# Kernel optimization log

Measured on AMD Instinct MI355X. Metric: run time of the kernel, lower is better.

## Reference

```python
import jax, jax.numpy as jnp
import numpy as np

B, N, CIN, H, OUT, E = 64, 512, 128, 256, 12, 8192


def setup_inputs() -> dict:
    key = jax.random.key(0)
    ks = jax.random.split(key, 32)
    g = lambda i, shape, s=0.05: jax.random.normal(ks[i], shape, jnp.float32) * s
    inp = {
        "x": jax.random.normal(ks[0], (B, N, CIN), jnp.float32),
        "edge_index": jax.random.randint(ks[1], (2, E), 0, N),
        "edge_weight": jax.random.uniform(ks[2], (E,), dtype=jnp.float32),
    }
    # TGCN2 gate params: GCNConv lin (CIN->H, bias added after aggregation) + Linear(2H->H)
    for j, gate in enumerate(["z", "r", "h"]):
        base = 3 + j * 4
        inp[f"W{gate}"] = g(base, (CIN, H))
        inp[f"b{gate}"] = jnp.zeros((H,), jnp.float32)
        inp[f"l{gate}_W"] = g(base + 1, (2 * H, H))
        inp[f"l{gate}_b"] = jnp.zeros((H,), jnp.float32)
    # 2-layer GRU (torch layout: W_ih [3H,in], W_hh [3H,H]); eval mode (dropout off)
    inp["Wih0"] = g(16, (3 * H, CIN)); inp["Whh0"] = g(17, (3 * H, H))
    inp["bih0"] = jnp.zeros((3 * H,), jnp.float32); inp["bhh0"] = jnp.zeros((3 * H,), jnp.float32)
    inp["Wih1"] = g(18, (3 * H, H)); inp["Whh1"] = g(19, (3 * H, H))
    inp["bih1"] = jnp.zeros((3 * H,), jnp.float32); inp["bhh1"] = jnp.zeros((3 * H,), jnp.float32)
    # heads (stored as [in,out] so y = x @ W + b, matching torch x @ W.T + b)
    inp["l1_W"] = g(20, (H, 1)); inp["l1_b"] = jnp.zeros((1,), jnp.float32)
    inp["l2_W"] = g(21, (H, 1)); inp["l2_b"] = jnp.zeros((1,), jnp.float32)
    inp["l3_W"] = g(22, (2, OUT)); inp["l3_b"] = jnp.zeros((OUT,), jnp.float32)
    return inp


def _gcn_norm(edge_index, edge_weight, n_nodes):
    # improved=True -> self loops with fill value 2.0; sym normalization
    loop = jnp.arange(n_nodes)
    src = jnp.concatenate([edge_index[0], loop])
    tgt = jnp.concatenate([edge_index[1], loop])
    ew = jnp.concatenate([edge_weight, jnp.full((n_nodes,), 2.0, edge_weight.dtype)])
    deg = jax.ops.segment_sum(ew, tgt, num_segments=n_nodes)
    dinv = jnp.where(deg > 0, deg ** -0.5, 0.0)
    return src, tgt, dinv[src] * ew * dinv[tgt]


def _gcn_conv(x, W, b, src, tgt, norm):
    xw = x @ W                                   # [B,N,H]
    msg = xw[:, src, :] * norm[None, :, None]    # gather from sources [B,E+N,H]
    out = jnp.zeros_like(xw).at[:, tgt, :].add(msg)  # scatter-add to targets
    return out + b


def _gru_layer(x_sbf, Wih, Whh, bih, bhh):
    h_dim = Whh.shape[1]
    h0 = jnp.zeros((x_sbf.shape[1], h_dim), x_sbf.dtype)

    def step(h, xt):
        gi = xt @ Wih.T + bih
        gh = h @ Whh.T + bhh
        ir, iz, inn = jnp.split(gi, 3, axis=-1)
        hr, hz, hn = jnp.split(gh, 3, axis=-1)
        r = jax.nn.sigmoid(ir + hr)
        z = jax.nn.sigmoid(iz + hz)
        n = jnp.tanh(inn + r * hn)
        h_new = (1.0 - z) * n + z * h
        return h_new, h_new

    _, ys = jax.lax.scan(step, h0, x_sbf)
    return ys  # [S,B,H]


def reference(x, edge_index, edge_weight, Wz, bz, lz_W, lz_b, Wr, br, lr_W, lr_b,
              Wh, bh, lh_W, lh_b, Wih0, Whh0, bih0, bhh0, Wih1, Whh1, bih1, bhh1,
              l1_W, l1_b, l2_W, l2_b, l3_W, l3_b):
    n_nodes = x.shape[1]
    # GRU branch (node dim treated as sequence, as in the source)
    xs = jnp.transpose(x, (1, 0, 2))             # [N,B,CIN]
    h1 = _gru_layer(xs, Wih0, Whh0, bih0, bhh0)
    h2 = _gru_layer(h1, Wih1, Whh1, bih1, bhh1)
    temp = jnp.transpose(h2, (1, 0, 2))          # [B,N,H]
    gru_out = temp @ l2_W + l2_b                 # [B,N,1]
    # TGCN2 cell with H0 = 0
    src, tgt, norm = _gcn_norm(edge_index, edge_weight, n_nodes)
    Hst = jnp.zeros((x.shape[0], n_nodes, lz_W.shape[1]), x.dtype)
    cz = _gcn_conv(x, Wz, bz, src, tgt, norm)
    Z = jax.nn.sigmoid(jnp.concatenate([cz, Hst], axis=2) @ lz_W + lz_b)
    cr = _gcn_conv(x, Wr, br, src, tgt, norm)
    R = jax.nn.sigmoid(jnp.concatenate([cr, Hst], axis=2) @ lr_W + lr_b)
    ch = _gcn_conv(x, Wh, bh, src, tgt, norm)
    H_tilde = jnp.tanh(jnp.concatenate([ch, Hst * R], axis=2) @ lh_W + lh_b)
    Hn = Z * Hst + (1.0 - Z) * H_tilde           # [B,N,H]
    h = jax.nn.relu(Hn) @ l1_W + l1_b            # [B,N,1]
    cat = jnp.concatenate([gru_out, h], axis=2)  # [B,N,2]
    return cat @ l3_W + l3_b                     # [B,N,OUT]
```

## Files before the change

### kernel.cpp

```cpp
#include <hip/hip_runtime.h>


typedef unsigned short u16;
typedef unsigned long long u64;
typedef short s8v __attribute__((ext_vector_type(8)));
typedef float f4v __attribute__((ext_vector_type(4)));

#define NBATCH 64
#define NNODE  512
#define DCIN   128
#define DHID   256
#define NEDGE  8192
#define RING   8
#define SLOTU16 16384

__device__ __forceinline__ u16 f2b(float f) {
    union { float f; unsigned int i; } v; v.f = f;
    unsigned int x = v.i;
    return (u16)((x + 0x7FFFu + ((x >> 16) & 1u)) >> 16);
}
__device__ __forceinline__ float sigm(float x)  { return 1.0f / (1.0f + __expf(-x)); }
__device__ __forceinline__ float tanh_(float x) { return 1.0f - 2.0f / (1.0f + __expf(2.0f * x)); }
__device__ __forceinline__ f4v mfma16(s8v a, s8v b, f4v c) {
    return __builtin_amdgcn_mfma_f32_16x16x32_bf16(a, b, c, 0, 0, 0);
}
__device__ __forceinline__ s8v ld_ring(const u64* p) {
    union { u64 d[2]; s8v v; } u;
    u.d[0] = __hip_atomic_load(p,     __ATOMIC_RELAXED, __HIP_MEMORY_SCOPE_AGENT);
    u.d[1] = __hip_atomic_load(p + 1, __ATOMIC_RELAXED, __HIP_MEMORY_SCOPE_AGENT);
    return u.v;
}
__device__ __forceinline__ void st_ring(u64* p, s8v v) {
    union { s8v v; u64 d[2]; } u; u.v = v;
    __hip_atomic_store(p,     u.d[0], __ATOMIC_RELAXED, __HIP_MEMORY_SCOPE_AGENT);
    __hip_atomic_store(p + 1, u.d[1], __ATOMIC_RELAXED, __HIP_MEMORY_SCOPE_AGENT);
}
__device__ __forceinline__ void wait_joint(const int* f, int tgtf,
                                           const int* g, int tgtg, int l) {
    while (true) {
        int v = 0x7fffffff, tg = -0x7fffffff;
        if (l < 16)      { v = __hip_atomic_load(f + l, __ATOMIC_RELAXED, __HIP_MEMORY_SCOPE_AGENT); tg = tgtf; }
        else if (l < 32) { v = __hip_atomic_load(g + (l - 16), __ATOMIC_RELAXED, __HIP_MEMORY_SCOPE_AGENT); tg = tgtg; }
        if (__all(v >= tg)) break;
        __builtin_amdgcn_s_sleep(2);
    }
    asm volatile("" ::: "memory");
}
__device__ __forceinline__ void wait_one(const int* f, int tgt, int l) {
    while (true) {
        int v = 0x7fffffff;
        if (l < 16) v = __hip_atomic_load(f + l, __ATOMIC_RELAXED, __HIP_MEMORY_SCOPE_AGENT);
        if (__all(v >= tgt)) break;
        __builtin_amdgcn_s_sleep(2);
    }
    asm volatile("" ::: "memory");
}
__device__ __forceinline__ s8v cvt8(const float* p) {
    s8v r;
    #pragma unroll
    for (int e = 0; e < 8; ++e) r[e] = (short)f2b(p[e]);
    return r;
}

__global__ void init_kernel(float* deg, int* counts, int* flags) {
    int i = blockIdx.x * blockDim.x + threadIdx.x;
    if (i < NNODE) { deg[i] = 2.0f; counts[i] = 1; }
    if (i < 128) flags[i] = 0;
}

__global__ void edge_deg_kernel(const int* __restrict__ ei, const float* __restrict__ ew,
                                float* deg, int* counts) {
    int e = blockIdx.x * blockDim.x + threadIdx.x;
    if (e < NEDGE) {
        int t = ei[NEDGE + e];
        atomicAdd(&deg[t], ew[e]);
        atomicAdd(&counts[t], 1);
    }
}

__global__ void scan_kernel(const float* __restrict__ deg, const int* __restrict__ counts,
                            float* __restrict__ dinv, int* __restrict__ rowptr,
                            int* __restrict__ cursor, int* __restrict__ col,
                            float* __restrict__ val) {
    __shared__ int sc[NNODE];
    int i = threadIdx.x;
    float d = deg[i];
    float di = (d > 0.0f) ? (1.0f / sqrtf(d)) : 0.0f;
    dinv[i] = di;
    int cnt = counts[i];
    sc[i] = cnt;
    __syncthreads();
    for (int ofs = 1; ofs < NNODE; ofs <<= 1) {
        int add = (i >= ofs) ? sc[i - ofs] : 0;
        __syncthreads();
        sc[i] += add;
        __syncthreads();
    }
    int ex = sc[i] - cnt;
    rowptr[i] = ex;
    if (i == NNODE - 1) rowptr[NNODE] = sc[NNODE - 1];
    col[ex] = i;
    val[ex] = di * 2.0f * di;
    cursor[i] = ex + 1;
}

__global__ void fill_kernel(const int* __restrict__ ei, const float* __restrict__ ew,
                            const float* __restrict__ dinv, int* cursor,
                            int* __restrict__ col, float* __restrict__ val) {
    int e = blockIdx.x * blockDim.x + threadIdx.x;
    if (e < NEDGE) {
        int s = ei[e], t = ei[NEDGE + e];
        int p = atomicAdd(&cursor[t], 1);
        col[p] = s;
        val[p] = dinv[s] * ew[e] * dinv[t];
    }
}

__global__ void fold_kernel(const float* __restrict__ Wz, const float* __restrict__ lzW,
                            const float* __restrict__ bz, const float* __restrict__ lzb,
                            const float* __restrict__ Wh, const float* __restrict__ lhW,
                            const float* __restrict__ bh, const float* __restrict__ lhb,
                            u16* __restrict__ Wf, float* __restrict__ bfold) {
    int nidx = blockIdx.x;
    int g = nidx & 1, j = nidx >> 1;
    int k = threadIdx.x;
    const float* W = g ? Wh : Wz;
    const float* L = g ? lhW : lzW;
    float acc = 0.0f;
    for (int m = 0; m < DHID; ++m)
        acc += W[k * DHID + m] * L[m * DHID + j];
    Wf[nidx * DCIN + k] = f2b(acc);
    if (k == 0) {
        const float* bg = g ? bh : bz;
        const float* lb = g ? lhb : lzb;
        float ab = 0.0f;
        for (int m = 0; m < DHID; ++m) ab += bg[m] * L[m * DHID + j];
        bfold[nidx] = ab + lb[j];
    }
}

__global__ void repack_w_kernel(const float* __restrict__ Wih, const float* __restrict__ Whh,
                                int KCX, int KC, int KX, int KH, u16* __restrict__ dst) {
    int id = blockIdx.x * 256 + threadIdx.x;
    int total = 16 * KC * 3 * 64;
    if (id >= total) return;
    int l = id & 63; int rest = id >> 6;
    int g = rest % 3; rest /= 3;
    int kc = rest % KC; rest /= KC;
    int r = rest;
    int j = r * 16 + (l & 15);
    int q = l >> 4;
    const float* src; int k;
    if (kc < KCX) { src = Wih + (size_t)(g * 256 + j) * KX; k = kc * 32 + q * 8; }
    else          { src = Whh + (size_t)(g * 256 + j) * KH; k = (kc - KCX) * 32 + q * 8; }
    u16* d = dst + (((size_t)(r * KC + kc)) * 3 + g) * 512 + l * 8;
    #pragma unroll
    for (int e = 0; e < 8; ++e) d[e] = f2b(src[k + e]);
}

__global__ __launch_bounds__(256)
void tgcn_kernel(const float* __restrict__ x, const int* __restrict__ rowptr,
                 const int* __restrict__ col, const float* __restrict__ val,
                 const u16* __restrict__ Wf, const float* __restrict__ bfold,
                 const float* __restrict__ l1W, float* __restrict__ hdot) {
    __shared__ u16 As[64][136];
    const int tid = threadIdx.x;
    const int bx = blockIdx.x;
    const int b = bx >> 3;
    const int n0 = (bx & 7) * 64;
    {
        const int c = tid & 127;
        const int half = tid >> 7;
        for (int it = 0; it < 32; ++it) {
            int r = it * 2 + half;
            int n = n0 + r;
            int s = rowptr[n], e = rowptr[n + 1];
            float acc = 0.0f;
            for (int i = s; i < e; ++i)
                acc += val[i] * x[((size_t)b * NNODE + col[i]) * DCIN + c];
            As[r][c] = f2b(acc);
        }
    }
    __syncthreads();
    const int w = tid >> 6, l = tid & 63;
    const int ncol = l & 15, q = l >> 4, ko = q * 8;
    s8v af[4];
    #pragma unroll
    for (int kc = 0; kc < 4; ++kc)
        af[kc] = *(const s8v*)(&As[w * 16 + ncol][kc * 32 + ko]);
    float partial[4] = {0.f, 0.f, 0.f, 0.f};
    for (int nc = 0; nc < 32; ++nc) {
        int n = nc * 16 + ncol;
        const u16* brow = Wf + (size_t)n * DCIN + ko;
        f4v acc = {0.f, 0.f, 0.f, 0.f};
        #pragma unroll
        for (int kc = 0; kc < 4; ++kc)
            acc = mfma16(af[kc], *(const s8v*)(brow + kc * 32), acc);
        float bias = bfold[n];
        float l1w = l1W[n >> 1];
        #pragma unroll
        for (int rr = 0; rr < 4; ++rr) {
            float v = acc[rr] + bias;
            float o = __shfl_xor(v, 1);
            float zpre = (ncol & 1) ? o : v;
            float hpre = (ncol & 1) ? v : o;
            float hn = (1.0f - sigm(zpre)) * tanh_(hpre);
            hn = hn > 0.0f ? hn : 0.0f;
            if (!(ncol & 1)) partial[rr] += hn * l1w;
        }
    }
    #pragma unroll
    for (int rr = 0; rr < 4; ++rr) {
        float p = partial[rr];
        p += __shfl_xor(p, 1); p += __shfl_xor(p, 2);
        p += __shfl_xor(p, 4); p += __shfl_xor(p, 8);
        if (ncol == 0)
            hdot[bx * 64 + w * 16 + q * 4 + rr] = p;
    }
}

__global__ __launch_bounds__(256)
void gru_pipe_kernel(const float* __restrict__ x,
                     const u16* __restrict__ Wpk0, const u16* __restrict__ Wpk1,
                     const float* __restrict__ bih0, const float* __restrict__ bhh0,
                     const float* __restrict__ bih1, const float* __restrict__ bhh1,
                     const float* __restrict__ l2W,
                     u16* __restrict__ h0ring, u16* __restrict__ h1ring,
                     int* flags, float* __restrict__ gpartg) {
    __shared__ u16 wlds[16 * 3 * 512];
    __shared__ u16 tile[4][16][16];

    const int tid = threadIdx.x;
    const int w = tid >> 6;
    const int l = tid & 63;
    const int q = l >> 4, ncol = l & 15;
    const bool isL1 = blockIdx.x >= 16;
    const int rblk = blockIdx.x & 15;
    const int KC = isL1 ? 16 : 12;

    int* fL0 = flags;
    int* fL1 = flags + 16;

    {
        const s8v* src = (const s8v*)((isL1 ? Wpk1 : Wpk0) + (size_t)rblk * KC * 3 * 512);
        s8v* dst = (s8v*)wlds;
        for (int i = tid; i < KC * 3 * 64; i += 256) dst[i] = src[i];
    }
    const int j = rblk * 16 + ncol;
    const float* bihp = isL1 ? bih1 : bih0;
    const float* bhhp = isL1 ? bhh1 : bhh0;
    const float br = bihp[j] + bhhp[j];
    const float bz = bihp[256 + j] + bhhp[256 + j];
    const float bi = bihp[512 + j];
    const float bhn = bhhp[512 + j];
    const float l2v = isL1 ? l2W[j] : 0.0f;
    float hreg[4] = {0.f, 0.f, 0.f, 0.f};
    const int qbase = 2 * (rblk & 1);
    u16* myring = isL1 ? h1ring : h0ring;
    const s8v* wf = (const s8v*)wlds;
    const float* xrow = x + ((size_t)(w * 16 + ncol) * NNODE) * DCIN + q * 8;
    __syncthreads();

    for (int t = 0; t < NNODE; ++t) {
        f4v accR = {0,0,0,0}, accZ = {0,0,0,0}, accNi = {0,0,0,0}, accNh = {0,0,0,0};
        if (!isL1) {
            const float* xp = xrow + (size_t)t * DCIN;
            #pragma unroll
            for (int kc = 0; kc < 4; ++kc) {
                s8v a = cvt8(xp + kc * 32);
                accR  = mfma16(a, wf[(kc * 3 + 0) * 64 + l], accR);
                accZ  = mfma16(a, wf[(kc * 3 + 1) * 64 + l], accZ);
                accNi = mfma16(a, wf[(kc * 3 + 2) * 64 + l], accNi);
            }
            wait_joint(fL0, t, fL1, t - 7, l);
            if (t > 0) {
                const u64* s1 = (const u64*)(h0ring + (size_t)((t - 1) & (RING - 1)) * SLOTU16);
                s8v a1[8];
                #pragma unroll
                for (int k = 0; k < 8; ++k)
                    a1[k] = ld_ring(s1 + (size_t)(w * 8 + k) * 128 + l * 2);
                #pragma unroll
                for (int k = 0; k < 8; ++k) {
                    int kc = 4 + k;
                    accR  = mfma16(a1[k], wf[(kc * 3 + 0) * 64 + l], accR);
                    accZ  = mfma16(a1[k], wf[(kc * 3 + 1) * 64 + l], accZ);
                    accNh = mfma16(a1[k], wf[(kc * 3 + 2) * 64 + l], accNh);
                }
            }
        } else {
            if (t > 0) {
                wait_one(fL1, t, l);
                const u64* s1 = (const u64*)(h1ring + (size_t)((t - 1) & (RING - 1)) * SLOTU16);
                s8v a1[8];
                #pragma unroll
                for (int k = 0; k < 8; ++k)
                    a1[k] = ld_ring(s1 + (size_t)(w * 8 + k) * 128 + l * 2);
                #pragma unroll
                for (int k = 0; k < 8; ++k) {
                    int kc = 8 + k;
                    accR  = mfma16(a1[k], wf[(kc * 3 + 0) * 64 + l], accR);
                    accZ  = mfma16(a1[k], wf[(kc * 3 + 1) * 64 + l], accZ);
                    accNh = mfma16(a1[k], wf[(kc * 3 + 2) * 64 + l], accNh);
                }
            }
            wait_one(fL0, t + 1, l);
            const u64* s0 = (const u64*)(h0ring + (size_t)(t & (RING - 1)) * SLOTU16);
            s8v a0[8];
            #pragma unroll
            for (int k = 0; k < 8; ++k)
                a0[k] = ld_ring(s0 + (size_t)(w * 8 + k) * 128 + l * 2);
            #pragma unroll
            for (int k = 0; k < 8; ++k) {
                accR  = mfma16(a0[k], wf[(k * 3 + 0) * 64 + l], accR);
                accZ  = mfma16(a0[k], wf[(k * 3 + 1) * 64 + l], accZ);
                accNi = mfma16(a0[k], wf[(k * 3 + 2) * 64 + l], accNi);
            }
        }
        float pd[4];
        #pragma unroll
        for (int rr = 0; rr < 4; ++rr) {
            float rv = sigm(accR[rr] + br);
            float zv = sigm(accZ[rr] + bz);
            float nv = tanh_(accNi[rr] + bi + rv * (accNh[rr] + bhn));
            float hn = nv + zv * (hreg[rr] - nv);
            hreg[rr] = hn;
            tile[w][q * 4 + rr][ncol] = f2b(hn);
            pd[rr] = hn * l2v;
        }
        if (isL1) {
            #pragma unroll
            for (int rr = 0; rr < 4; ++rr) {
                float v = pd[rr];
                v += __shfl_xor(v, 1); v += __shfl_xor(v, 2);
                v += __shfl_xor(v, 4); v += __shfl_xor(v, 8);
                if (ncol == 0)
                    gpartg[((size_t)t * 16 + rblk) * 64 + w * 16 + q * 4 + rr] = v;
            }
        }
        if (q == qbase || q == qbase + 1) {
            s8v v = *(const s8v*)&tile[w][ncol][8 * (q - qbase)];
            u64* dst = (u64*)(myring + (size_t)(t & (RING - 1)) * SLOTU16)
                       + (size_t)(w * 8 + (rblk >> 1)) * 128 + l * 2;
            st_ring(dst, v);
        }
        __syncthreads();
        if (tid == 0)
            __hip_atomic_store((isL1 ? fL1 : fL0) + rblk, t + 1,
                               __ATOMIC_RELAXED, __HIP_MEMORY_SCOPE_AGENT);
    }
}

__global__ __launch_bounds__(256)
void head_kernel(const float* __restrict__ gpartg, const float* __restrict__ hdot,
                 const float* __restrict__ l1b, const float* __restrict__ l2b,
                 const float* __restrict__ l3W, const float* __restrict__ l3b,
                 float* __restrict__ out) {
    int idx = blockIdx.x * 256 + threadIdx.x;
    if (idx >= NBATCH * NNODE * 12) return;
    int r = idx / 12, oc = idx - r * 12;
    int b = r >> 9, n = r & 511;
    float g = 0.0f;
    #pragma unroll
    for (int k = 0; k < 16; ++k) g += gpartg[((size_t)n * 16 + k) * 64 + b];
    g += l2b[0];
    float hh = hdot[r] + l1b[0];
    out[idx] = g * l3W[oc] + hh * l3W[12 + oc] + l3b[oc];
}

static hipStream_t g_side = nullptr;
static hipEvent_t  g_evA  = nullptr;
static hipEvent_t  g_evB  = nullptr;
namespace {
struct SideInit {
    SideInit() {
        if (hipStreamCreateWithFlags(&g_side, hipStreamNonBlocking) != hipSuccess) g_side = nullptr;
        if (hipEventCreateWithFlags(&g_evA, hipEventDisableTiming) != hipSuccess) g_evA = nullptr;
        if (hipEventCreateWithFlags(&g_evB, hipEventDisableTiming) != hipSuccess) g_evB = nullptr;
    }
};
static SideInit g_side_init;
}

extern "C" void kernel_launch(void* const* d_in, const int* in_sizes, int n_in,
                              void* d_out, int out_size, void* d_ws, size_t ws_size,
                              hipStream_t stream) {
    const float* x    = (const float*)d_in[0];
    const int*   ei   = (const int*)  d_in[1];
    const float* ew   = (const float*)d_in[2];
    const float* Wz   = (const float*)d_in[3];
    const float* bz   = (const float*)d_in[4];
    const float* lzW  = (const float*)d_in[5];
    const float* lzb  = (const float*)d_in[6];
    const float* Wh   = (const float*)d_in[11];
    const float* bh   = (const float*)d_in[12];
    const float* lhW  = (const float*)d_in[13];
    const float* lhb  = (const float*)d_in[14];
    const float* Wih0 = (const float*)d_in[15];
    const float* Whh0 = (const float*)d_in[16];
    const float* bih0 = (const float*)d_in[17];
    const float* bhh0 = (const float*)d_in[18];
    const float* Wih1 = (const float*)d_in[19];
    const float* Whh1 = (const float*)d_in[20];
    const float* bih1 = (const float*)d_in[21];
    const float* bhh1 = (const float*)d_in[22];
    const float* l1W  = (const float*)d_in[23];
    const float* l1b  = (const float*)d_in[24];
    const float* l2W  = (const float*)d_in[25];
    const float* l2b  = (const float*)d_in[26];
    const float* l3W  = (const float*)d_in[27];
    const float* l3b  = (const float*)d_in[28];

    char* ws = (char*)d_ws;
    size_t o = 0;
    auto take = [&](size_t nbytes) {
        char* p = ws + o;
        o = (o + nbytes + 255) & ~(size_t)255;
        return p;
    };
    float* deg    = (float*)take(NNODE * 4);
    float* dinv   = (float*)take(NNODE * 4);
    int*   rowptr = (int*)  take((NNODE + 1) * 4);
    int*   cursor = (int*)  take(NNODE * 4);
    int*   col    = (int*)  take((NEDGE + NNODE) * 4);
    float* val    = (float*)take((NEDGE + NNODE) * 4);
    u16*   Wf     = (u16*)  take((size_t)512 * DCIN * 2);
    float* bfold  = (float*)take(512 * 4);
    float* hdot   = (float*)take((size_t)NBATCH * NNODE * 4);
    float* gpartg = (float*)take((size_t)NNODE * 16 * 64 * 4);
    u16*   Wpk0   = (u16*)  take((size_t)16 * 12 * 3 * 512 * 2);
    u16*   Wpk1   = (u16*)  take((size_t)16 * 16 * 3 * 512 * 2);
    u16*   h0ring = (u16*)  take((size_t)RING * SLOTU16 * 2);
    u16*   h1ring = (u16*)  take((size_t)RING * SLOTU16 * 2);
    int*   flags  = (int*)  take(512);
    if (o > ws_size) return;

    const bool fork = (g_side && g_evA && g_evB);
    hipStream_t sideS = fork ? g_side : stream;

    init_kernel<<<2, 256, 0, stream>>>(deg, cursor, flags);

    if (fork) {
        hipEventRecord(g_evA, stream);
        hipStreamWaitEvent(sideS, g_evA, 0);
    }

    edge_deg_kernel<<<NEDGE / 256, 256, 0, sideS>>>(ei, ew, deg, cursor);
    scan_kernel<<<1, NNODE, 0, sideS>>>(deg, cursor, dinv, rowptr, cursor, col, val);
    fill_kernel<<<NEDGE / 256, 256, 0, sideS>>>(ei, ew, dinv, cursor, col, val);
    fold_kernel<<<512, DCIN, 0, sideS>>>(Wz, lzW, bz, lzb, Wh, lhW, bh, lhb, Wf, bfold);
    tgcn_kernel<<<512, 256, 0, sideS>>>(x, rowptr, col, val, Wf, bfold, l1W, hdot);
    if (fork) hipEventRecord(g_evB, sideS);

    repack_w_kernel<<<(16 * 12 * 3 * 64 + 255) / 256, 256, 0, stream>>>(
        Wih0, Whh0, 4, 12, DCIN, DHID, Wpk0);
    repack_w_kernel<<<(16 * 16 * 3 * 64 + 255) / 256, 256, 0, stream>>>(
        Wih1, Whh1, 8, 16, DHID, DHID, Wpk1);
    gru_pipe_kernel<<<32, 256, 0, stream>>>(x, Wpk0, Wpk1, bih0, bhh0,
                                            bih1, bhh1, l2W, h0ring, h1ring,
                                            flags, gpartg);

    if (fork) hipStreamWaitEvent(stream, g_evB, 0);
    head_kernel<<<(NBATCH * NNODE * 12 + 255) / 256, 256, 0, stream>>>(
        gpartg, hdot, l1b, l2b, l3W, l3b, (float*)d_out);
    (void)in_sizes; (void)n_in; (void)out_size;
}
```

Measured before the change: 2.374 ms.

## Replace per-block step flags with per-wave stamps in GRU pipeline

Each wave now publishes its ring-slot data and then writes a per-slot, per-wave stamp right after its own store, instead of waiting for a block-wide barrier and a single per-block flag. Consumers wait only on the stamps for the batch rows their wave reads. This is meant to cut the latency on the serial recurrence critical path between the layer-0 and layer-1 blocks. The per-block flag is kept for layer-1 back-pressure on layer 0. The change relies on relaxed atomics plus a vmcnt wait for ordering, which carries a memory-visibility risk, and the stamp buffer grows.

```diff
diff --git a/kernel.cpp b/kernel.cpp
--- a/kernel.cpp
+++ b/kernel.cpp
@@ -35,22 +35,22 @@
     __hip_atomic_store(p,     u.d[0], __ATOMIC_RELAXED, __HIP_MEMORY_SCOPE_AGENT);
     __hip_atomic_store(p + 1, u.d[1], __ATOMIC_RELAXED, __HIP_MEMORY_SCOPE_AGENT);
 }
-__device__ __forceinline__ void wait_joint(const int* f, int tgtf,
-                                           const int* g, int tgtg, int l) {
+__device__ __forceinline__ void wait_stamp(const int* sp, int tgt, int l) {
+    while (true) {
+        int v = 0x7fffffff;
+        if (l < 16) v = __hip_atomic_load(sp + l, __ATOMIC_RELAXED, __HIP_MEMORY_SCOPE_AGENT);
+        if (__all(v >= tgt)) break;
+        __builtin_amdgcn_s_sleep(2);
+    }
+    asm volatile("" ::: "memory");
+}
+__device__ __forceinline__ void wait_stamp_slack(const int* sp, int tgt,
+                                                 const int* fp, int tgtf, int l) {
     while (true) {
         int v = 0x7fffffff, tg = -0x7fffffff;
-        if (l < 16)      { v = __hip_atomic_load(f + l, __ATOMIC_RELAXED, __HIP_MEMORY_SCOPE_AGENT); tg = tgtf; }
-        else if (l < 32) { v = __hip_atomic_load(g + (l - 16), __ATOMIC_RELAXED, __HIP_MEMORY_SCOPE_AGENT); tg = tgtg; }
+        if (l < 16)      { v = __hip_atomic_load(sp + l, __ATOMIC_RELAXED, __HIP_MEMORY_SCOPE_AGENT); tg = tgt; }
+        else if (l < 32) { v = __hip_atomic_load(fp + (l - 16), __ATOMIC_RELAXED, __HIP_MEMORY_SCOPE_AGENT); tg = tgtf; }
         if (__all(v >= tg)) break;
-        __builtin_amdgcn_s_sleep(2);
-    }
-    asm volatile("" ::: "memory");
-}
-__device__ __forceinline__ void wait_one(const int* f, int tgt, int l) {
-    while (true) {
-        int v = 0x7fffffff;
-        if (l < 16) v = __hip_atomic_load(f + l, __ATOMIC_RELAXED, __HIP_MEMORY_SCOPE_AGENT);
-        if (__all(v >= tgt)) break;
         __builtin_amdgcn_s_sleep(2);
     }
     asm volatile("" ::: "memory");
@@ -62,10 +62,10 @@
     return r;
 }
 
-__global__ void init_kernel(float* deg, int* counts, int* flags) {
+__global__ void init_kernel(float* deg, int* counts, int* syncb) {
     int i = blockIdx.x * blockDim.x + threadIdx.x;
     if (i < NNODE) { deg[i] = 2.0f; counts[i] = 1; }
-    if (i < 128) flags[i] = 0;
+    if (i < 2048) syncb[i] = 0;
 }
 
 __global__ void edge_deg_kernel(const int* __restrict__ ei, const float* __restrict__ ew,
@@ -226,7 +226,7 @@
                      const float* __restrict__ bih1, const float* __restrict__ bhh1,
                      const float* __restrict__ l2W,
                      u16* __restrict__ h0ring, u16* __restrict__ h1ring,
-                     int* flags, float* __restrict__ gpartg) {
+                     int* syncb, float* __restrict__ gpartg) {
     __shared__ u16 wlds[16 * 3 * 512];
     __shared__ u16 tile[4][16][16];
 
@@ -238,8 +238,9 @@
     const int rblk = blockIdx.x & 15;
     const int KC = isL1 ? 16 : 12;
 
-    int* fL0 = flags;
-    int* fL1 = flags + 16;
+    int* fL1 = syncb + 16;
+    int* st0 = syncb + 64;
+    int* st1 = syncb + 64 + 512;
 
     {
         const s8v* src = (const s8v*)((isL1 ? Wpk1 : Wpk0) + (size_t)rblk * KC * 3 * 512);
@@ -257,11 +258,14 @@
     float hreg[4] = {0.f, 0.f, 0.f, 0.f};
     const int qbase = 2 * (rblk & 1);
     u16* myring = isL1 ? h1ring : h0ring;
+    int* myst = isL1 ? st1 : st0;
+    int* myflag = (isL1 ? fL1 : syncb) + rblk;
     const s8v* wf = (const s8v*)wlds;
     const float* xrow = x + ((size_t)(w * 16 + ncol) * NNODE) * DCIN + q * 8;
     __syncthreads();
 
     for (int t = 0; t < NNODE; ++t) {
+        const int scur = t & (RING - 1), sprev = (t - 1) & (RING - 1);
         f4v accR = {0,0,0,0}, accZ = {0,0,0,0}, accNi = {0,0,0,0}, accNh = {0,0,0,0};
         if (!isL1) {
             const float* xp = xrow + (size_t)t * DCIN;
@@ -272,9 +276,9 @@
                 accZ  = mfma16(a, wf[(kc * 3 + 1) * 64 + l], accZ);
                 accNi = mfma16(a, wf[(kc * 3 + 2) * 64 + l], accNi);
             }
-            wait_joint(fL0, t, fL1, t - 7, l);
             if (t > 0) {
-                const u64* s1 = (const u64*)(h0ring + (size_t)((t - 1) & (RING - 1)) * SLOTU16);
+                wait_stamp_slack(st0 + sprev * 64 + w * 16, t, fL1, t - 7, l);
+                const u64* s1 = (const u64*)(h0ring + (size_t)sprev * SLOTU16);
                 s8v a1[8];
                 #pragma unroll
                 for (int k = 0; k < 8; ++k)
@@ -288,9 +292,21 @@
                 }
             }
         } else {
+            wait_stamp(st0 + scur * 64 + w * 16, t + 1, l);
+            const u64* s0 = (const u64*)(h0ring + (size_t)scur * SLOTU16);
+            s8v a0[8];
+            #pragma unroll
+            for (int k = 0; k < 8; ++k)
+                a0[k] = ld_ring(s0 + (size_t)(w * 8 + k) * 128 + l * 2);
+            #pragma unroll
+            for (int k = 0; k < 8; ++k) {
+                accR  = mfma16(a0[k], wf[(k * 3 + 0) * 64 + l], accR);
+                accZ  = mfma16(a0[k], wf[(k * 3 + 1) * 64 + l], accZ);
+                accNi = mfma16(a0[k], wf[(k * 3 + 2) * 64 + l], accNi);
+            }
             if (t > 0) {
-                wait_one(fL1, t, l);
-                const u64* s1 = (const u64*)(h1ring + (size_t)((t - 1) & (RING - 1)) * SLOTU16);
+                wait_stamp(st1 + sprev * 64 + w * 16, t, l);
+                const u64* s1 = (const u64*)(h1ring + (size_t)sprev * SLOTU16);
                 s8v a1[8];
                 #pragma unroll
                 for (int k = 0; k < 8; ++k)
@@ -303,18 +319,6 @@
                     accNh = mfma16(a1[k], wf[(kc * 3 + 2) * 64 + l], accNh);
                 }
             }
-            wait_one(fL0, t + 1, l);
-            const u64* s0 = (const u64*)(h0ring + (size_t)(t & (RING - 1)) * SLOTU16);
-            s8v a0[8];
-            #pragma unroll
-            for (int k = 0; k < 8; ++k)
-                a0[k] = ld_ring(s0 + (size_t)(w * 8 + k) * 128 + l * 2);
-            #pragma unroll
-            for (int k = 0; k < 8; ++k) {
-                accR  = mfma16(a0[k], wf[(k * 3 + 0) * 64 + l], accR);
-                accZ  = mfma16(a0[k], wf[(k * 3 + 1) * 64 + l], accZ);
-                accNi = mfma16(a0[k], wf[(k * 3 + 2) * 64 + l], accNi);
-            }
         }
         float pd[4];
         #pragma unroll
@@ -327,6 +331,16 @@
             tile[w][q * 4 + rr][ncol] = f2b(hn);
             pd[rr] = hn * l2v;
         }
+        if (q == qbase || q == qbase + 1) {
+            s8v v = *(const s8v*)&tile[w][ncol][8 * (q - qbase)];
+            u64* dst = (u64*)(myring + (size_t)scur * SLOTU16)
+                       + (size_t)(w * 8 + (rblk >> 1)) * 128 + l * 2;
+            st_ring(dst, v);
+        }
+        asm volatile("s_waitcnt vmcnt(0)" ::: "memory");
+        if (l == 0)
+            __hip_atomic_store(myst + scur * 64 + w * 16 + rblk, t + 1,
+                               __ATOMIC_RELAXED, __HIP_MEMORY_SCOPE_AGENT);
         if (isL1) {
             #pragma unroll
             for (int rr = 0; rr < 4; ++rr) {
@@ -337,15 +351,9 @@
                     gpartg[((size_t)t * 16 + rblk) * 64 + w * 16 + q * 4 + rr] = v;
             }
         }
-        if (q == qbase || q == qbase + 1) {
-            s8v v = *(const s8v*)&tile[w][ncol][8 * (q - qbase)];
-            u64* dst = (u64*)(myring + (size_t)(t & (RING - 1)) * SLOTU16)
-                       + (size_t)(w * 8 + (rblk >> 1)) * 128 + l * 2;
-            st_ring(dst, v);
-        }
         __syncthreads();
         if (tid == 0)
-            __hip_atomic_store((isL1 ? fL1 : fL0) + rblk, t + 1,
+            __hip_atomic_store(myflag, t + 1,
                                __ATOMIC_RELAXED, __HIP_MEMORY_SCOPE_AGENT);
     }
 }
@@ -431,13 +439,13 @@
     u16*   Wpk1   = (u16*)  take((size_t)16 * 16 * 3 * 512 * 2);
     u16*   h0ring = (u16*)  take((size_t)RING * SLOTU16 * 2);
     u16*   h1ring = (u16*)  take((size_t)RING * SLOTU16 * 2);
-    int*   flags  = (int*)  take(512);
+    int*   syncb  = (int*)  take(8192);
     if (o > ws_size) return;
 
     const bool fork = (g_side && g_evA && g_evB);
     hipStream_t sideS = fork ? g_side : stream;
 
-    init_kernel<<<2, 256, 0, stream>>>(deg, cursor, flags);
+    init_kernel<<<8, 256, 0, stream>>>(deg, cursor, syncb);
 
     if (fork) {
         hipEventRecord(g_evA, stream);
@@ -457,7 +465,7 @@
         Wih1, Whh1, 8, 16, DHID, DHID, Wpk1);
     gru_pipe_kernel<<<32, 256, 0, stream>>>(x, Wpk0, Wpk1, bih0, bhh0,
                                             bih1, bhh1, l2W, h0ring, h1ring,
-                                            flags, gpartg);
+                                            syncb, gpartg);
 
     if (fork) hipStreamWaitEvent(stream, g_evB, 0);
     head_kernel<<<(NBATCH * NNODE * 12 + 255) / 256, 256, 0, stream>>>(
```

Result: faster. 2.277 ms (-4.1%).
